# Kernel optimization log

Hardware: AMD Instinct MI355X
Metric: run time of the kernel (lower is better)

Reference implementation:

```python
import jax, jax.numpy as jnp
import numpy as np


def setup_inputs() -> dict:
    key = jax.random.key(0)
    k0, k1, k2, k3, k4 = jax.random.split(key, 5)
    T, B, S, H = 32, 8192, 256, 128
    return {
        "states_batch": jax.random.normal(k0, (T, B, S), dtype=jnp.float32),
        "W1": jax.random.normal(k1, (T, S, H), dtype=jnp.float32) * (S ** -0.5),
        "b1": jax.random.normal(k2, (T, H), dtype=jnp.float32) * 0.01,
        "W2": jax.random.normal(k3, (T, H, 1), dtype=jnp.float32) * 0.01,
        "b2": jax.random.normal(k4, (T, 1), dtype=jnp.float32) * 0.01,
    }


def reference(states_batch, W1, b1, W2, b2):
    # [T,B,S] @ [T,S,H] -> [T,B,H], bias, SiLU
    h = jnp.einsum('tbs,tsh->tbh', states_batch, W1) + b1[:, None, :]
    h = jax.nn.silu(h)
    # [T,B,H] @ [T,H,1] -> [T,B,1], bias, squeeze -> [T,B]
    out = jnp.einsum('tbh,tho->tbo', h, W2) + b2[:, None, :]
    return out.squeeze(-1)
```

## Files before the change

### kernel.cpp

```cpp
#include <hip/hip_runtime.h>
#include <hip/hip_bf16.h>

typedef __attribute__((ext_vector_type(8))) short bf16x8;
typedef __attribute__((ext_vector_type(4))) float f32x4;

#define T_DIM 32
#define B_DIM 8192
#define S_DIM 256
#define H_DIM 128
#define BM    32
#define NCH   16
#define BLOCKS_PER_T 16

__device__ __forceinline__ uint32_t cvt_pk_bf16(float lo, float hi) {
  uint32_t r;
  asm("v_cvt_pk_bf16_f32 %0, %1, %2" : "=v"(r) : "v"(lo), "v"(hi));
  return r;
}

#define BARRIER() asm volatile("s_waitcnt lgkmcnt(0)\n\ts_barrier" ::: "memory")

#define ISSUE8(av, c)                                                          \
  _Pragma("unroll")                                                            \
  for (int j = 0; j < 8; ++j)                                                  \
    av[j] = __builtin_nontemporal_load(&A4[(size_t)(c) * 2048 + j * 256 + tid]);

#define CONVERT8(av, LDSBUF)                                                   \
  _Pragma("unroll")                                                            \
  for (int j = 0; j < 8; ++j) {                                                \
    const int f   = j * 256 + tid;                                             \
    const int row = f >> 6;                                                    \
    const int kq  = f & 63;                                                    \
    const uint32_t lo = cvt_pk_bf16(av[j].x, av[j].y);                         \
    const uint32_t hi = cvt_pk_bf16(av[j].z, av[j].w);                         \
    const int byteoff = (row * 512 + kq * 8) ^ ((row & 7) << 4);               \
    *reinterpret_cast<uint2*>(&(LDSBUF)[byteoff]) = make_uint2(lo, hi);        \
  }

#define MFMA_EPI(LDSBUF, RI)                                                   \
  {                                                                            \
    f32x4 acc[2][2];                                                           \
    _Pragma("unroll")                                                          \
    for (int mt = 0; mt < 2; ++mt) {                                           \
      acc[mt][0] = (f32x4){0.f, 0.f, 0.f, 0.f};                                \
      acc[mt][1] = (f32x4){0.f, 0.f, 0.f, 0.f};                                \
    }                                                                          \
    _Pragma("unroll")                                                          \
    for (int mt = 0; mt < 2; ++mt) {                                           \
      const int row = mt * 16 + l15;                                           \
      bf16x8 afr[8];                                                           \
      _Pragma("unroll")                                                        \
      for (int ks = 0; ks < 8; ++ks) {                                         \
        const int byteoff =                                                    \
            (row * 512 + ks * 64 + lg * 16) ^ ((row & 7) << 4);                \
        afr[ks] = *reinterpret_cast<const bf16x8*>(&(LDSBUF)[byteoff]);        \
      }                                                                        \
      _Pragma("unroll")                                                        \
      for (int ks = 0; ks < 8; ++ks) {                                         \
        acc[mt][0] = __builtin_amdgcn_mfma_f32_16x16x32_bf16(                  \
            afr[ks], bfr[0][ks], acc[mt][0], 0, 0, 0);                         \
        acc[mt][1] = __builtin_amdgcn_mfma_f32_16x16x32_bf16(                  \
            afr[ks], bfr[1][ks], acc[mt][1], 0, 0, 0);                         \
      }                                                                        \
    }                                                                          \
    _Pragma("unroll")                                                          \
    for (int mt = 0; mt < 2; ++mt) {                                           \
      float part[4];                                                           \
      _Pragma("unroll")                                                        \
      for (int r = 0; r < 4; ++r) {                                            \
        float s = 0.f;                                                         \
        _Pragma("unroll")                                                      \
        for (int nloc = 0; nloc < 2; ++nloc) {                                 \
          const float h   = acc[mt][nloc][r] + b1c[nloc];                      \
          const float sig = 1.f / (1.f + __expf(-h));                          \
          s += h * sig * w2c[nloc];                                            \
        }                                                                      \
        s += __shfl_xor(s, 1);                                                 \
        s += __shfl_xor(s, 2);                                                 \
        s += __shfl_xor(s, 4);                                                 \
        s += __shfl_xor(s, 8);                                                 \
        part[r] = s;                                                           \
      }                                                                        \
      if (l15 == 0) {                                                          \
        _Pragma("unroll")                                                      \
        for (int r = 0; r < 4; ++r)                                            \
          red[RI][wid][mt * 16 + lg * 4 + r] = part[r];                        \
      }                                                                        \
    }                                                                          \
  }

#define OUTW(RI, cc)                                                           \
  if (tid < BM) {                                                              \
    const float o = red[RI][0][tid] + red[RI][1][tid] + red[RI][2][tid] +      \
                    red[RI][3][tid] + b2t;                                     \
    __builtin_nontemporal_store(o, &outw[(cc) * BM + tid]);                    \
  }

__global__ __launch_bounds__(256, 2) void cvar_mlp_kernel(
    const float* __restrict__ states, const float* __restrict__ W1,
    const float* __restrict__ b1, const float* __restrict__ W2,
    const float* __restrict__ b2, float* __restrict__ out)
{
  __shared__ __align__(16) char ldsA[2][BM * 512];
  __shared__ float red[2][4][BM];

  const int tid  = threadIdx.x;
  const int wid  = tid >> 6;
  const int lane = tid & 63;
  const int l15  = lane & 15;
  const int lg   = lane >> 4;

  const int bidx = blockIdx.x;
  const int xcd  = bidx & 7;
  const int slot = bidx >> 3;
  const int t    = xcd * 4 + (slot >> 4);
  const int cg   = slot & 15;
  const int b0   = cg * (BM * NCH);

  const float* Ag  = states + ((size_t)t * B_DIM + b0) * S_DIM;
  const f32x4* A4  = reinterpret_cast<const f32x4*>(Ag);
  const float* W1g = W1 + (size_t)t * (S_DIM * H_DIM);
  float*      outw = out + (size_t)t * B_DIM + b0;

  f32x4 avA[8], avB[8];
  ISSUE8(avA, 0);
  ISSUE8(avB, 1);

  bf16x8 bfr[2][8];
#pragma unroll
  for (int nloc = 0; nloc < 2; ++nloc) {
    const int ncol = (wid * 2 + nloc) * 16 + l15;
#pragma unroll
    for (int ks = 0; ks < 8; ++ks) {
      const int kbase = ks * 32 + lg * 8;
      float e[8];
#pragma unroll
      for (int j = 0; j < 8; ++j)
        e[j] = W1g[(size_t)(kbase + j) * H_DIM + ncol];
      union { uint32_t u[4]; bf16x8 v; } uu;
      uu.u[0] = cvt_pk_bf16(e[0], e[1]);
      uu.u[1] = cvt_pk_bf16(e[2], e[3]);
      uu.u[2] = cvt_pk_bf16(e[4], e[5]);
      uu.u[3] = cvt_pk_bf16(e[6], e[7]);
      bfr[nloc][ks] = uu.v;
    }
  }

  float b1c[2], w2c[2];
#pragma unroll
  for (int nloc = 0; nloc < 2; ++nloc) {
    const int col = (wid * 2 + nloc) * 16 + l15;
    b1c[nloc] = b1[(size_t)t * H_DIM + col];
    w2c[nloc] = W2[(size_t)t * H_DIM + col];
  }
  const float b2t = b2[t];

  CONVERT8(avA, ldsA[0]);
  ISSUE8(avA, 2);
  BARRIER();

#pragma unroll 1
  for (int c = 0; c < NCH; c += 2) {
    MFMA_EPI(ldsA[0], 0);
    if (c + 1 < NCH) {
      CONVERT8(avB, ldsA[1]);
      if (c + 3 < NCH) ISSUE8(avB, c + 3);
    }
    BARRIER();
    OUTW(0, c);

    MFMA_EPI(ldsA[1], 1);
    if (c + 2 < NCH) {
      CONVERT8(avA, ldsA[0]);
      if (c + 4 < NCH) ISSUE8(avA, c + 4);
    }
    BARRIER();
    OUTW(1, c + 1);
  }
}

extern "C" void kernel_launch(void* const* d_in, const int* in_sizes, int n_in,
                              void* d_out, int out_size, void* d_ws, size_t ws_size,
                              hipStream_t stream) {
  const float* states = (const float*)d_in[0];
  const float* W1     = (const float*)d_in[1];
  const float* b1     = (const float*)d_in[2];
  const float* W2     = (const float*)d_in[3];
  const float* b2     = (const float*)d_in[4];
  float* out          = (float*)d_out;

  const int grid = T_DIM * BLOCKS_PER_T;
  cvar_mlp_kernel<<<grid, 256, 0, stream>>>(states, W1, b1, W2, b2, out);
}
```

Baseline: 65.57 us.

## Double grid size, single register prefetch buffer, raise occupancy to four blocks/CU

Halves the chunks per block and doubles the block count. The two-deep register prefetch of states is cut to a single buffer, and A fragments are loaded from LDS per k-step instead of all eight up front. Launch bounds rise to four blocks per SM so more waves can hide memory latency. Nontemporal loads and stores become plain accesses. The cost is less in-flight prefetch per wave and twice as many per-block W1 loads.

New measurement: 194.5 us. +196.6%, slower.

```diff
diff --git a/kernel.cpp b/kernel.cpp
--- a/kernel.cpp
+++ b/kernel.cpp
@@ -9,8 +9,8 @@
 #define S_DIM 256
 #define H_DIM 128
 #define BM    32
-#define NCH   16
-#define BLOCKS_PER_T 16
+#define NCH   8
+#define BLOCKS_PER_T 32
 
 __device__ __forceinline__ uint32_t cvt_pk_bf16(float lo, float hi) {
   uint32_t r;
@@ -23,7 +23,7 @@
 #define ISSUE8(av, c)                                                          \
   _Pragma("unroll")                                                            \
   for (int j = 0; j < 8; ++j)                                                  \
-    av[j] = __builtin_nontemporal_load(&A4[(size_t)(c) * 2048 + j * 256 + tid]);
+    av[j] = A4[(size_t)(c) * 2048 + j * 256 + tid];
 
 #define CONVERT8(av, LDSBUF)                                                   \
   _Pragma("unroll")                                                            \
@@ -48,19 +48,16 @@
     _Pragma("unroll")                                                          \
     for (int mt = 0; mt < 2; ++mt) {                                           \
       const int row = mt * 16 + l15;                                           \
-      bf16x8 afr[8];                                                           \
       _Pragma("unroll")                                                        \
       for (int ks = 0; ks < 8; ++ks) {                                         \
         const int byteoff =                                                    \
             (row * 512 + ks * 64 + lg * 16) ^ ((row & 7) << 4);                \
-        afr[ks] = *reinterpret_cast<const bf16x8*>(&(LDSBUF)[byteoff]);        \
-      }                                                                        \
-      _Pragma("unroll")                                                        \
-      for (int ks = 0; ks < 8; ++ks) {                                         \
+        const bf16x8 afr =                                                     \
+            *reinterpret_cast<const bf16x8*>(&(LDSBUF)[byteoff]);              \
         acc[mt][0] = __builtin_amdgcn_mfma_f32_16x16x32_bf16(                  \
-            afr[ks], bfr[0][ks], acc[mt][0], 0, 0, 0);                         \
+            afr, bfr[0][ks], acc[mt][0], 0, 0, 0);                             \
         acc[mt][1] = __builtin_amdgcn_mfma_f32_16x16x32_bf16(                  \
-            afr[ks], bfr[1][ks], acc[mt][1], 0, 0, 0);                         \
+            afr, bfr[1][ks], acc[mt][1], 0, 0, 0);                             \
       }                                                                        \
     }                                                                          \
     _Pragma("unroll")                                                          \
@@ -93,10 +90,10 @@
   if (tid < BM) {                                                              \
     const float o = red[RI][0][tid] + red[RI][1][tid] + red[RI][2][tid] +      \
                     red[RI][3][tid] + b2t;                                     \
-    __builtin_nontemporal_store(o, &outw[(cc) * BM + tid]);                    \
+    outw[(cc) * BM + tid] = o;                                                 \
   }
 
-__global__ __launch_bounds__(256, 2) void cvar_mlp_kernel(
+__global__ __launch_bounds__(256, 4) void cvar_mlp_kernel(
     const float* __restrict__ states, const float* __restrict__ W1,
     const float* __restrict__ b1, const float* __restrict__ W2,
     const float* __restrict__ b2, float* __restrict__ out)
@@ -113,8 +110,8 @@
   const int bidx = blockIdx.x;
   const int xcd  = bidx & 7;
   const int slot = bidx >> 3;
-  const int t    = xcd * 4 + (slot >> 4);
-  const int cg   = slot & 15;
+  const int t    = xcd * 4 + (slot >> 5);
+  const int cg   = slot & 31;
   const int b0   = cg * (BM * NCH);
 
   const float* Ag  = states + ((size_t)t * B_DIM + b0) * S_DIM;
@@ -122,9 +119,8 @@
   const float* W1g = W1 + (size_t)t * (S_DIM * H_DIM);
   float*      outw = out + (size_t)t * B_DIM + b0;
 
-  f32x4 avA[8], avB[8];
-  ISSUE8(avA, 0);
-  ISSUE8(avB, 1);
+  f32x4 av[8];
+  ISSUE8(av, 0);
 
   bf16x8 bfr[2][8];
 #pragma unroll
@@ -155,24 +151,22 @@
   }
   const float b2t = b2[t];
 
-  CONVERT8(avA, ldsA[0]);
-  ISSUE8(avA, 2);
+  CONVERT8(av, ldsA[0]);
+  ISSUE8(av, 1);
   BARRIER();
 
 #pragma unroll 1
   for (int c = 0; c < NCH; c += 2) {
     MFMA_EPI(ldsA[0], 0);
-    if (c + 1 < NCH) {
-      CONVERT8(avB, ldsA[1]);
-      if (c + 3 < NCH) ISSUE8(avB, c + 3);
-    }
+    CONVERT8(av, ldsA[1]);
+    if (c + 2 < NCH) ISSUE8(av, c + 2);
     BARRIER();
     OUTW(0, c);
 
     MFMA_EPI(ldsA[1], 1);
     if (c + 2 < NCH) {
-      CONVERT8(avA, ldsA[0]);
-      if (c + 4 < NCH) ISSUE8(avA, c + 4);
+      CONVERT8(av, ldsA[0]);
+      if (c + 3 < NCH) ISSUE8(av, c + 3);
     }
     BARRIER();
     OUTW(1, c + 1);
```
